# Kernel tuning notes

Measured on AMD Instinct MI355X. Metric: run time of the kernel, lower is better.

The kernel has to match this reference:

```python
import jax, jax.numpy as jnp
import numpy as np

HIDDEN = 512
HEAD = 64
SEQ = 2048
CHUNK = 256
GAMMA = 0.96875
SCALE_BASE = 512.0


def _xpos(x, downscale):
    # x: [B, L, hd]; XPOS with offset=0 (scale rows == length, no trimming needed)
    B, L, hd = x.shape
    half = hd // 2
    scale_vec = (jnp.arange(0, hd, 2, dtype=jnp.float32) + 0.4 * hd) / (1.4 * hd)  # [half]
    power = jnp.arange(L, dtype=jnp.float32) / SCALE_BASE                          # [L]
    scale = scale_vec[None, :] ** power[:, None]                                   # [L, half]
    inv_freq = 1.0 / (10000.0 ** (jnp.arange(half, dtype=jnp.float32) / half))
    sinusoid = jnp.arange(L, dtype=jnp.float32)[:, None] * inv_freq[None, :]       # [L, half]
    sin, cos = jnp.sin(sinusoid), jnp.cos(sinusoid)
    if downscale:
        scale = 1.0 / scale
    # duplicate_interleave: repeat each column twice -> [L, hd]
    sin_f = jnp.repeat(sin * scale, 2, axis=-1)
    cos_f = jnp.repeat(cos * scale, 2, axis=-1)
    x1 = x[:, :, 0::2]
    x2 = x[:, :, 1::2]
    rot = jnp.stack((-x2, x1), axis=-1).reshape(B, L, hd)  # rotate_every_two
    return x * cos_f + rot * sin_f


def _D_parallel():
    # D[i, j] = gamma^|i-j| if j < (i//chunk + 1)*chunk else 0 (block-causal with in-chunk lookahead)
    i = jnp.arange(SEQ)[:, None]
    j = jnp.arange(SEQ)[None, :]
    j_max = (i // CHUNK + 1) * CHUNK
    decay = GAMMA ** jnp.abs(i - j).astype(jnp.float32)
    return jnp.where(j < j_max, decay, 0.0)  # gamma>0 so no NaNs to scrub


def setup_inputs() -> dict:
    key = jax.random.key(0)
    k1, k2, k3, k4 = jax.random.split(key, 4)
    X = jax.random.normal(k1, (8, SEQ, HIDDEN), dtype=jnp.float32)
    W_Q = jax.random.normal(k2, (HIDDEN, HEAD), dtype=jnp.float32) / HIDDEN
    W_K = jax.random.normal(k3, (HIDDEN, HEAD), dtype=jnp.float32) / HIDDEN
    W_V = jax.random.normal(k4, (HIDDEN, HEAD), dtype=jnp.float32) / HIDDEN
    return {"X": X, "W_Q": W_Q, "W_K": W_K, "W_V": W_V}


def reference(X, W_Q, W_K, W_V):
    Q = _xpos(X @ W_Q, downscale=False)   # [B, S, H]
    K = _xpos(X @ W_K, downscale=True)    # [B, S, H]
    V = X @ W_V                           # [B, S, V]
    D = _D_parallel()                     # [S, S]
    scores = jnp.einsum('bqh,bkh->bqk', Q, K) * D[None]
    return jnp.einsum('bqk,bkv->bqv', scores, V)
```

## Files before the change

### kernel.cpp

```cpp
#include <hip/hip_runtime.h>
#include <hip/hip_bf16.h>


typedef __attribute__((ext_vector_type(8))) short short8;
typedef __attribute__((ext_vector_type(4))) float floatx4;

#define LOG2GAMMA (-0.04580350f)
#define GINV      (1.0f / 0.96875f)

static __device__ __forceinline__ unsigned short f2bf(float f) {
    __hip_bfloat16 h = __float2bfloat16(f);
    return *reinterpret_cast<unsigned short*>(&h);
}


__global__ __launch_bounds__(256) void prep_kernel(
    const float* __restrict__ Wq, const float* __restrict__ Wk,
    const float* __restrict__ Wv,
    __hip_bfloat16* __restrict__ Wfrag, float* __restrict__ tabs)
{
    int idx = blockIdx.x * 256 + threadIdx.x;
    const int WF_N = 192 * 512;
    if (idx < WF_N) {
        int j    = idx & 7;
        int n15  = (idx >> 3) & 15;
        int quad = (idx >> 7) & 3;
        int kkg  = (idx >> 9) & 15;
        int tile = idx >> 13;
        int n = tile * 16 + n15;
        int k = kkg * 32 + quad * 8 + j;
        int m = n >> 6, c = n & 63;
        const float* W = (m == 0) ? Wq : ((m == 1) ? Wk : Wv);
        Wfrag[idx] = __float2bfloat16(W[k * 64 + c]);
    } else {
        int t2 = idx - WF_N;
        if (t2 < 4 * 2048 * 32) {
            int tab = t2 >> 16;
            int rem = t2 & 65535;
            int pos = rem >> 5;
            int t   = rem & 31;
            float inv_freq = powf(10000.0f, -(float)t / 32.0f);
            float sinus = (float)pos * inv_freq;
            float s = sinf(sinus), c = cosf(sinus);
            float sv = (2.0f * (float)t + 0.4f * 64.0f) / (1.4f * 64.0f);
            float power = (float)pos / 512.0f;
            float scl = powf(sv, (tab >= 2) ? -power : power);
            tabs[t2] = ((tab & 1) == 0) ? c * scl : s * scl;
        }
    }
}

__global__ __launch_bounds__(256, 4) void proj_kernel(
    const float* __restrict__ X, const __hip_bfloat16* __restrict__ Wfrag,
    const float* __restrict__ tabs,
    __hip_bfloat16* __restrict__ Qfrag, __hip_bfloat16* __restrict__ Kfrag,
    __hip_bfloat16* __restrict__ Vfrag, __hip_bfloat16* __restrict__ Qsfrag,
    __hip_bfloat16* __restrict__ Ktfrag)
{
    __shared__ __hip_bfloat16 smem[32 * 520];

    int tid = threadIdx.x;
    int r0 = blockIdx.x * 32;
    int w = tid >> 6, lane = tid & 63, quad = lane >> 4, l15 = lane & 15;
    int rh = w & 1, nh = w >> 1;

#pragma unroll
    for (int u = 0; u < 16; u++) {
        int f = u * 256 + tid;
        int row = f >> 7, c = f & 127;
        float4 v = *(const float4*)(X + (r0 + row) * 512 + c * 4);
        ushort4 pk;
        pk.x = f2bf(v.x); pk.y = f2bf(v.y); pk.z = f2bf(v.z); pk.w = f2bf(v.w);
        *(ushort4*)&smem[row * 520 + c * 4] = pk;
    }
    __syncthreads();

    floatx4 acc[6];
#pragma unroll
    for (int t = 0; t < 6; t++) acc[t] = (floatx4){0.f, 0.f, 0.f, 0.f};

#pragma unroll
    for (int ks = 0; ks < 16; ks++) {
        short8 a = *(const short8*)&smem[(rh * 16 + l15) * 520 + ks * 32 + quad * 8];
#pragma unroll
        for (int t = 0; t < 6; t++) {
            int tile = nh * 6 + t;
            short8 bfr = *(const short8*)(Wfrag + ((tile * 16 + ks) * 64 + lane) * 8);
            acc[t] = __builtin_amdgcn_mfma_f32_16x16x32_bf16(a, bfr, acc[t], 0, 0, 0);
        }
    }
    __syncthreads();

    __hip_bfloat16* bufQ  = smem;
    __hip_bfloat16* bufK  = smem + 2304;
    __hip_bfloat16* bufV  = smem + 4608;
    __hip_bfloat16* bufQs = smem + 7168;
    int b = r0 >> 11, n0 = r0 & 2047;
    int rrow = rh * 16 + quad * 4;

#pragma unroll
    for (int tl = 0; tl < 6; tl++) {
        int t = nh * 6 + tl;
#pragma unroll
        for (int rg = 0; rg < 4; rg++) {
            int row = rrow + rg;
            int n = n0 + row;
            float val = acc[tl][rg];
            float prt = __shfl_xor(val, 1, 64);
            if (t < 4) {
                int ch = t * 16 + l15, tt = ch >> 1;
                float co = tabs[n * 32 + tt];
                float si = tabs[65536 + n * 32 + tt];
                float o = (l15 & 1) ? (val * co + prt * si) : (val * co - prt * si);
                bufQ[row * 72 + ch] = __float2bfloat16(o);
                float qs = exp2f(LOG2GAMMA * (float)((n & 255) + 1));
                bufQs[row * 72 + ch] = __float2bfloat16(o * qs);
            } else if (t < 8) {
                int ch = (t - 4) * 16 + l15, tt = ch >> 1;
                float co = tabs[131072 + n * 32 + tt];
                float si = tabs[196608 + n * 32 + tt];
                float o = (l15 & 1) ? (val * co + prt * si) : (val * co - prt * si);
                bufK[row * 72 + ch] = __float2bfloat16(o);
            } else {
                int ch = (t - 8) * 16 + l15;
                bufV[ch * 40 + row] = __float2bfloat16(val);
            }
        }
    }
    __syncthreads();

    {
        int tile2 = tid >> 7, kk = (tid >> 6) & 1, ln = tid & 63;
        int q2 = ln >> 4, m15 = ln & 15;
        size_t qkbase = ((((size_t)b * 128 + (n0 >> 4) + tile2) * 2 + kk) * 64 + ln) * 8;
        uint4 vq = *(const uint4*)&bufQ[(tile2 * 16 + m15) * 72 + kk * 32 + q2 * 8];
        *(uint4*)(Qfrag + qkbase) = vq;
        uint4 vqs = *(const uint4*)&bufQs[(tile2 * 16 + m15) * 72 + kk * 32 + q2 * 8];
        *(uint4*)(Qsfrag + qkbase) = vqs;
        uint4 vk = *(const uint4*)&bufK[(tile2 * 16 + m15) * 72 + kk * 32 + q2 * 8];
        *(uint4*)(Kfrag + qkbase) = vk;
        int t2 = tid >> 6;
        uint4 vv = *(const uint4*)&bufV[(t2 * 16 + m15) * 40 + q2 * 8];
        *(uint4*)(Vfrag + ((((size_t)b * 64 + (n0 >> 5)) * 4 + t2) * 64 + ln) * 8) = vv;
    }
    {
        int wdt = tid >> 6, ln2 = tid & 63;
        int q2 = ln2 >> 4, m15 = ln2 & 15;
        int jb0 = (n0 & 255) + q2 * 8;
        float sc = exp2f(LOG2GAMMA * (float)(255 - jb0));
        short8 pk;
#pragma unroll
        for (int jj = 0; jj < 8; jj++) {
            float v = __bfloat162float(bufK[(q2 * 8 + jj) * 72 + wdt * 16 + m15]) * sc;
            pk[jj] = (short)f2bf(v);
            sc *= GINV;
        }
        int c = n0 >> 8, ksg = (n0 >> 5) & 7;
        *(short8*)(Ktfrag + ((((size_t)(b * 8 + c) * 4 + wdt) * 8 + ksg) * 64 + ln2) * 8) = pk;
    }
}

__global__ __launch_bounds__(256, 2) void zk_kernel(
    const __hip_bfloat16* __restrict__ Ktfrag,
    const __hip_bfloat16* __restrict__ Vfrag, float* __restrict__ Zf)
{
    __shared__ float zz[64 * 68];

    int tid = threadIdx.x;
    int b = blockIdx.x >> 3, c = blockIdx.x & 7;
    int w = tid >> 6, lane = tid & 63, quad = lane >> 4, l15 = lane & 15;

    floatx4 acc[4];
#pragma unroll
    for (int t = 0; t < 4; t++) acc[t] = (floatx4){0.f, 0.f, 0.f, 0.f};

#pragma unroll
    for (int ks = 0; ks < 8; ks++) {
        short8 a = *(const short8*)(Ktfrag +
            ((((size_t)(b * 8 + c) * 4 + w) * 8 + ks) * 64 + lane) * 8);
#pragma unroll
        for (int vt = 0; vt < 4; vt++) {
            short8 bfr = *(const short8*)(Vfrag +
                ((((size_t)b * 64 + c * 8 + ks) * 4 + vt) * 64 + lane) * 8);
            acc[vt] = __builtin_amdgcn_mfma_f32_16x16x32_bf16(a, bfr, acc[vt], 0, 0, 0);
        }
    }
#pragma unroll
    for (int vt = 0; vt < 4; vt++)
#pragma unroll
        for (int rg = 0; rg < 4; rg++)
            zz[(w * 16 + quad * 4 + rg) * 68 + vt * 16 + l15] = acc[vt][rg];
    __syncthreads();

    {
        int vt = tid >> 6;
#pragma unroll
        for (int kk = 0; kk < 2; kk++) {
            float v[8];
#pragma unroll
            for (int jd = 0; jd < 8; jd++)
                v[jd] = zz[(kk * 32 + quad * 8 + jd) * 68 + vt * 16 + l15];
            float* zp = Zf + (((((size_t)(b * 8 + c) * 4 + vt) * 2 + kk) * 64 + lane) * 8);
            *(float4*)zp       = (float4){v[0], v[1], v[2], v[3]};
            *(float4*)(zp + 4) = (float4){v[4], v[5], v[6], v[7]};
        }
    }
}

__global__ __launch_bounds__(128, 4) void attn_kernel(
    const __hip_bfloat16* __restrict__ Qfrag, const __hip_bfloat16* __restrict__ Kfrag,
    const __hip_bfloat16* __restrict__ Vfrag, const __hip_bfloat16* __restrict__ Qsfrag,
    const float* __restrict__ Zf, float* __restrict__ out)
{
    __shared__ __hip_bfloat16 P[2 * 16 * 132];
    __shared__ float obuf[16 * 68];

    int tid = threadIdx.x;
    int b = blockIdx.x >> 7, qt = blockIdx.x & 127;
    int qc = qt >> 4;
    int h = tid >> 6, lane = tid & 63, quad = lane >> 4, l15 = lane & 15;
    __hip_bfloat16* Pw = P + h * 2112;

    short8 qf[2];
#pragma unroll
    for (int kk = 0; kk < 2; kk++)
        qf[kk] = *(const short8*)(Qfrag + (((size_t)(b * 128 + qt) * 2 + kk) * 64 + lane) * 8);

    floatx4 o[4];
#pragma unroll
    for (int t = 0; t < 4; t++) o[t] = (floatx4){0.f, 0.f, 0.f, 0.f};

    int il0 = (qt & 15) * 16 + quad * 4;

#pragma unroll
    for (int g = 0; g < 2; g++) {
        floatx4 s[4];
#pragma unroll
        for (int t = 0; t < 4; t++) s[t] = (floatx4){0.f, 0.f, 0.f, 0.f};
#pragma unroll
        for (int t = 0; t < 4; t++) {
            int kt = qc * 16 + h * 8 + g * 4 + t;
#pragma unroll
            for (int kk = 0; kk < 2; kk++) {
                short8 bfr = *(const short8*)(Kfrag +
                    (((size_t)(b * 128 + kt) * 2 + kk) * 64 + lane) * 8);
                s[t] = __builtin_amdgcn_mfma_f32_16x16x32_bf16(qf[kk], bfr, s[t], 0, 0, 0);
            }
        }
#pragma unroll
        for (int t = 0; t < 4; t++) {
            int jl = h * 128 + (g * 4 + t) * 16 + l15;
#pragma unroll
            for (int rg = 0; rg < 4; rg++) {
                int d = il0 + rg - jl; d = (d < 0) ? -d : d;
                float p = s[t][rg] * exp2f(LOG2GAMMA * (float)d);
                Pw[(quad * 4 + rg) * 132 + (g * 4 + t) * 16 + l15] = __float2bfloat16(p);
            }
        }
    }
#pragma unroll
    for (int ks = 0; ks < 4; ks++) {
        short8 a = *(const short8*)&Pw[l15 * 132 + ks * 32 + quad * 8];
#pragma unroll
        for (int vt = 0; vt < 4; vt++) {
            short8 bfr = *(const short8*)(Vfrag +
                ((((size_t)b * 64 + qc * 8 + h * 4 + ks) * 4 + vt) * 64 + lane) * 8);
            o[vt] = __builtin_amdgcn_mfma_f32_16x16x32_bf16(a, bfr, o[vt], 0, 0, 0);
        }
    }

    if (qc > 0) {
        short8 aq = *(const short8*)(Qsfrag +
            (((size_t)(b * 128 + qt) * 2 + h) * 64 + lane) * 8);
        int nz = (qc < 3) ? qc : 3;
        float cm0 = 1.0f;
        float cm1 = exp2f(LOG2GAMMA * 256.0f);
        float cm2 = exp2f(LOG2GAMMA * 512.0f);
#pragma unroll
        for (int vt = 0; vt < 4; vt++) {
            float hv[8];
#pragma unroll
            for (int jd = 0; jd < 8; jd++) hv[jd] = 0.f;
            for (int m = 0; m < nz; m++) {
                float cm = (m == 0) ? cm0 : ((m == 1) ? cm1 : cm2);
                const float* zp = Zf +
                    (((((size_t)(b * 8 + qc - 1 - m) * 4 + vt) * 2 + h) * 64 + lane) * 8);
                float4 z0 = *(const float4*)zp;
                float4 z1 = *(const float4*)(zp + 4);
                hv[0] += cm * z0.x; hv[1] += cm * z0.y;
                hv[2] += cm * z0.z; hv[3] += cm * z0.w;
                hv[4] += cm * z1.x; hv[5] += cm * z1.y;
                hv[6] += cm * z1.z; hv[7] += cm * z1.w;
            }
            short8 hb;
#pragma unroll
            for (int jd = 0; jd < 8; jd++) hb[jd] = (short)f2bf(hv[jd]);
            o[vt] = __builtin_amdgcn_mfma_f32_16x16x32_bf16(aq, hb, o[vt], 0, 0, 0);
        }
    }

    if (h == 1) {
#pragma unroll
        for (int vt = 0; vt < 4; vt++)
#pragma unroll
            for (int rg = 0; rg < 4; rg++)
                obuf[(quad * 4 + rg) * 68 + vt * 16 + l15] = o[vt][rg];
    }
    __syncthreads();
    if (h == 0) {
        int rbase = b * 2048 + qt * 16 + quad * 4;
#pragma unroll
        for (int vt = 0; vt < 4; vt++)
#pragma unroll
            for (int rg = 0; rg < 4; rg++)
                out[(size_t)(rbase + rg) * 64 + vt * 16 + l15] =
                    o[vt][rg] + obuf[(quad * 4 + rg) * 68 + vt * 16 + l15];
    }
}

extern "C" void kernel_launch(void* const* d_in, const int* in_sizes, int n_in,
                              void* d_out, int out_size, void* d_ws, size_t ws_size,
                              hipStream_t stream) {
    const float* X  = (const float*)d_in[0];
    const float* Wq = (const float*)d_in[1];
    const float* Wk = (const float*)d_in[2];
    const float* Wv = (const float*)d_in[3];
    float* out = (float*)d_out;

    char* ws = (char*)d_ws;
    __hip_bfloat16* Wfrag  = (__hip_bfloat16*)(ws);
    float*          tabs   = (float*)(ws + 196608);
    __hip_bfloat16* Qfrag  = (__hip_bfloat16*)(ws + 1245184);
    __hip_bfloat16* Kfrag  = (__hip_bfloat16*)(ws + 3342336);
    __hip_bfloat16* Vfrag  = (__hip_bfloat16*)(ws + 5439488);
    __hip_bfloat16* Qsfrag = (__hip_bfloat16*)(ws + 7536640);
    __hip_bfloat16* Ktfrag = (__hip_bfloat16*)(ws + 9633792);
    float*          Zf     = (float*)(ws + 11730944);

    prep_kernel<<<1408, 256, 0, stream>>>(Wq, Wk, Wv, Wfrag, tabs);
    proj_kernel<<<512, 256, 0, stream>>>(X, Wfrag, tabs, Qfrag, Kfrag, Vfrag,
                                         Qsfrag, Ktfrag);
    zk_kernel<<<64, 256, 0, stream>>>(Ktfrag, Vfrag, Zf);
    attn_kernel<<<1024, 128, 0, stream>>>(Qfrag, Kfrag, Vfrag, Qsfrag, Zf, out);
}
```

Measured before the change: 111.8 us.

## Drop Qs buffer, split zk over key halves, reuse A fragments in projection

Removes the separately stored decay-scaled Q copy. The cross-chunk term now uses the plain Q fragment and applies the per-row decay scale to the accumulator afterwards, which cuts proj_kernel stores and attn_kernel loads. The projection kernel has each wave cover both 16-row halves with 3 weight tiles, so each weight fragment load feeds two MFMAs. zk_kernel is split over two key halves to double its grid, and attn_kernel now reads and sums twice as many Z partials in exchange.

```diff
diff --git a/kernel.cpp b/kernel.cpp
--- a/kernel.cpp
+++ b/kernel.cpp
@@ -54,15 +54,13 @@
     const float* __restrict__ X, const __hip_bfloat16* __restrict__ Wfrag,
     const float* __restrict__ tabs,
     __hip_bfloat16* __restrict__ Qfrag, __hip_bfloat16* __restrict__ Kfrag,
-    __hip_bfloat16* __restrict__ Vfrag, __hip_bfloat16* __restrict__ Qsfrag,
-    __hip_bfloat16* __restrict__ Ktfrag)
+    __hip_bfloat16* __restrict__ Vfrag, __hip_bfloat16* __restrict__ Ktfrag)
 {
     __shared__ __hip_bfloat16 smem[32 * 520];
 
     int tid = threadIdx.x;
     int r0 = blockIdx.x * 32;
-    int w = tid >> 6, lane = tid & 63, quad = lane >> 4, l15 = lane & 15;
-    int rh = w & 1, nh = w >> 1;
+    int nh = tid >> 6, lane = tid & 63, quad = lane >> 4, l15 = lane & 15;
 
 #pragma unroll
     for (int u = 0; u < 16; u++) {
@@ -81,49 +79,50 @@
 
 #pragma unroll
     for (int ks = 0; ks < 16; ks++) {
-        short8 a = *(const short8*)&smem[(rh * 16 + l15) * 520 + ks * 32 + quad * 8];
-#pragma unroll
-        for (int t = 0; t < 6; t++) {
-            int tile = nh * 6 + t;
+        short8 a0 = *(const short8*)&smem[l15 * 520 + ks * 32 + quad * 8];
+        short8 a1 = *(const short8*)&smem[(16 + l15) * 520 + ks * 32 + quad * 8];
+#pragma unroll
+        for (int tl = 0; tl < 3; tl++) {
+            int tile = nh * 3 + tl;
             short8 bfr = *(const short8*)(Wfrag + ((tile * 16 + ks) * 64 + lane) * 8);
-            acc[t] = __builtin_amdgcn_mfma_f32_16x16x32_bf16(a, bfr, acc[t], 0, 0, 0);
-        }
-    }
-    __syncthreads();
-
-    __hip_bfloat16* bufQ  = smem;
-    __hip_bfloat16* bufK  = smem + 2304;
-    __hip_bfloat16* bufV  = smem + 4608;
-    __hip_bfloat16* bufQs = smem + 7168;
+            acc[tl * 2 + 0] = __builtin_amdgcn_mfma_f32_16x16x32_bf16(a0, bfr, acc[tl * 2 + 0], 0, 0, 0);
+            acc[tl * 2 + 1] = __builtin_amdgcn_mfma_f32_16x16x32_bf16(a1, bfr, acc[tl * 2 + 1], 0, 0, 0);
+        }
+    }
+    __syncthreads();
+
+    __hip_bfloat16* bufQ = smem;
+    __hip_bfloat16* bufK = smem + 2304;
+    __hip_bfloat16* bufV = smem + 4608;
     int b = r0 >> 11, n0 = r0 & 2047;
-    int rrow = rh * 16 + quad * 4;
-
-#pragma unroll
-    for (int tl = 0; tl < 6; tl++) {
-        int t = nh * 6 + tl;
-#pragma unroll
-        for (int rg = 0; rg < 4; rg++) {
-            int row = rrow + rg;
-            int n = n0 + row;
-            float val = acc[tl][rg];
-            float prt = __shfl_xor(val, 1, 64);
-            if (t < 4) {
-                int ch = t * 16 + l15, tt = ch >> 1;
-                float co = tabs[n * 32 + tt];
-                float si = tabs[65536 + n * 32 + tt];
-                float o = (l15 & 1) ? (val * co + prt * si) : (val * co - prt * si);
-                bufQ[row * 72 + ch] = __float2bfloat16(o);
-                float qs = exp2f(LOG2GAMMA * (float)((n & 255) + 1));
-                bufQs[row * 72 + ch] = __float2bfloat16(o * qs);
-            } else if (t < 8) {
-                int ch = (t - 4) * 16 + l15, tt = ch >> 1;
-                float co = tabs[131072 + n * 32 + tt];
-                float si = tabs[196608 + n * 32 + tt];
-                float o = (l15 & 1) ? (val * co + prt * si) : (val * co - prt * si);
-                bufK[row * 72 + ch] = __float2bfloat16(o);
-            } else {
-                int ch = (t - 8) * 16 + l15;
-                bufV[ch * 40 + row] = __float2bfloat16(val);
+
+#pragma unroll
+    for (int tl = 0; tl < 3; tl++) {
+        int t = nh * 3 + tl;
+#pragma unroll
+        for (int r = 0; r < 2; r++) {
+#pragma unroll
+            for (int rg = 0; rg < 4; rg++) {
+                int row = r * 16 + quad * 4 + rg;
+                int n = n0 + row;
+                float val = acc[tl * 2 + r][rg];
+                float prt = __shfl_xor(val, 1, 64);
+                if (t < 4) {
+                    int ch = t * 16 + l15, tt = ch >> 1;
+                    float co = tabs[n * 32 + tt];
+                    float si = tabs[65536 + n * 32 + tt];
+                    float o = (l15 & 1) ? (val * co + prt * si) : (val * co - prt * si);
+                    bufQ[row * 72 + ch] = __float2bfloat16(o);
+                } else if (t < 8) {
+                    int ch = (t - 4) * 16 + l15, tt = ch >> 1;
+                    float co = tabs[131072 + n * 32 + tt];
+                    float si = tabs[196608 + n * 32 + tt];
+                    float o = (l15 & 1) ? (val * co + prt * si) : (val * co - prt * si);
+                    bufK[row * 72 + ch] = __float2bfloat16(o);
+                } else {
+                    int ch = (t - 8) * 16 + l15;
+                    bufV[ch * 40 + row] = __float2bfloat16(val);
+                }
             }
         }
     }
@@ -135,8 +134,6 @@
         size_t qkbase = ((((size_t)b * 128 + (n0 >> 4) + tile2) * 2 + kk) * 64 + ln) * 8;
         uint4 vq = *(const uint4*)&bufQ[(tile2 * 16 + m15) * 72 + kk * 32 + q2 * 8];
         *(uint4*)(Qfrag + qkbase) = vq;
-        uint4 vqs = *(const uint4*)&bufQs[(tile2 * 16 + m15) * 72 + kk * 32 + q2 * 8];
-        *(uint4*)(Qsfrag + qkbase) = vqs;
         uint4 vk = *(const uint4*)&bufK[(tile2 * 16 + m15) * 72 + kk * 32 + q2 * 8];
         *(uint4*)(Kfrag + qkbase) = vk;
         int t2 = tid >> 6;
@@ -167,7 +164,7 @@
     __shared__ float zz[64 * 68];
 
     int tid = threadIdx.x;
-    int b = blockIdx.x >> 3, c = blockIdx.x & 7;
+    int b = blockIdx.x >> 4, c = (blockIdx.x >> 1) & 7, kh = blockIdx.x & 1;
     int w = tid >> 6, lane = tid & 63, quad = lane >> 4, l15 = lane & 15;
 
     floatx4 acc[4];
@@ -175,13 +172,14 @@
     for (int t = 0; t < 4; t++) acc[t] = (floatx4){0.f, 0.f, 0.f, 0.f};
 
 #pragma unroll
-    for (int ks = 0; ks < 8; ks++) {
+    for (int ks = 0; ks < 4; ks++) {
+        int ksg = kh * 4 + ks;
         short8 a = *(const short8*)(Ktfrag +
-            ((((size_t)(b * 8 + c) * 4 + w) * 8 + ks) * 64 + lane) * 8);
+            ((((size_t)(b * 8 + c) * 4 + w) * 8 + ksg) * 64 + lane) * 8);
 #pragma unroll
         for (int vt = 0; vt < 4; vt++) {
             short8 bfr = *(const short8*)(Vfrag +
-                ((((size_t)b * 64 + c * 8 + ks) * 4 + vt) * 64 + lane) * 8);
+                ((((size_t)b * 64 + c * 8 + ksg) * 4 + vt) * 64 + lane) * 8);
             acc[vt] = __builtin_amdgcn_mfma_f32_16x16x32_bf16(a, bfr, acc[vt], 0, 0, 0);
         }
     }
@@ -200,7 +198,8 @@
 #pragma unroll
             for (int jd = 0; jd < 8; jd++)
                 v[jd] = zz[(kk * 32 + quad * 8 + jd) * 68 + vt * 16 + l15];
-            float* zp = Zf + (((((size_t)(b * 8 + c) * 4 + vt) * 2 + kk) * 64 + lane) * 8);
+            float* zp = Zf +
+                ((((((size_t)(b * 8 + c) * 2 + kh) * 4 + vt) * 2 + kk) * 64 + lane) * 8);
             *(float4*)zp       = (float4){v[0], v[1], v[2], v[3]};
             *(float4*)(zp + 4) = (float4){v[4], v[5], v[6], v[7]};
         }
@@ -209,8 +208,8 @@
 
 __global__ __launch_bounds__(128, 4) void attn_kernel(
     const __hip_bfloat16* __restrict__ Qfrag, const __hip_bfloat16* __restrict__ Kfrag,
-    const __hip_bfloat16* __restrict__ Vfrag, const __hip_bfloat16* __restrict__ Qsfrag,
-    const float* __restrict__ Zf, float* __restrict__ out)
+    const __hip_bfloat16* __restrict__ Vfrag, const float* __restrict__ Zf,
+    float* __restrict__ out)
 {
     __shared__ __hip_bfloat16 P[2 * 16 * 132];
     __shared__ float obuf[16 * 68];
@@ -270,10 +269,10 @@
     }
 
     if (qc > 0) {
-        short8 aq = *(const short8*)(Qsfrag +
-            (((size_t)(b * 128 + qt) * 2 + h) * 64 + lane) * 8);
+        floatx4 oc[4];
+#pragma unroll
+        for (int t = 0; t < 4; t++) oc[t] = (floatx4){0.f, 0.f, 0.f, 0.f};
         int nz = (qc < 3) ? qc : 3;
-        float cm0 = 1.0f;
         float cm1 = exp2f(LOG2GAMMA * 256.0f);
         float cm2 = exp2f(LOG2GAMMA * 512.0f);
 #pragma unroll
@@ -282,21 +281,33 @@
 #pragma unroll
             for (int jd = 0; jd < 8; jd++) hv[jd] = 0.f;
             for (int m = 0; m < nz; m++) {
-                float cm = (m == 0) ? cm0 : ((m == 1) ? cm1 : cm2);
-                const float* zp = Zf +
-                    (((((size_t)(b * 8 + qc - 1 - m) * 4 + vt) * 2 + h) * 64 + lane) * 8);
-                float4 z0 = *(const float4*)zp;
-                float4 z1 = *(const float4*)(zp + 4);
-                hv[0] += cm * z0.x; hv[1] += cm * z0.y;
-                hv[2] += cm * z0.z; hv[3] += cm * z0.w;
-                hv[4] += cm * z1.x; hv[5] += cm * z1.y;
-                hv[6] += cm * z1.z; hv[7] += cm * z1.w;
+                float cm = (m == 0) ? 1.0f : ((m == 1) ? cm1 : cm2);
+#pragma unroll
+                for (int kh = 0; kh < 2; kh++) {
+                    const float* zp = Zf +
+                        ((((((size_t)(b * 8 + qc - 1 - m) * 2 + kh) * 4 + vt) * 2 + h) * 64 + lane) * 8);
+                    float4 z0 = *(const float4*)zp;
+                    float4 z1 = *(const float4*)(zp + 4);
+                    hv[0] += cm * z0.x; hv[1] += cm * z0.y;
+                    hv[2] += cm * z0.z; hv[3] += cm * z0.w;
+                    hv[4] += cm * z1.x; hv[5] += cm * z1.y;
+                    hv[6] += cm * z1.z; hv[7] += cm * z1.w;
+                }
             }
             short8 hb;
 #pragma unroll
             for (int jd = 0; jd < 8; jd++) hb[jd] = (short)f2bf(hv[jd]);
-            o[vt] = __builtin_amdgcn_mfma_f32_16x16x32_bf16(aq, hb, o[vt], 0, 0, 0);
-        }
+            oc[vt] = __builtin_amdgcn_mfma_f32_16x16x32_bf16(qf[h], hb, oc[vt], 0, 0, 0);
+        }
+        float rs[4];
+#pragma unroll
+        for (int rg = 0; rg < 4; rg++)
+            rs[rg] = exp2f(LOG2GAMMA * (float)(il0 + rg + 1));
+#pragma unroll
+        for (int vt = 0; vt < 4; vt++)
+#pragma unroll
+            for (int rg = 0; rg < 4; rg++)
+                o[vt][rg] += oc[vt][rg] * rs[rg];
     }
 
     if (h == 1) {
@@ -333,13 +344,11 @@
     __hip_bfloat16* Qfrag  = (__hip_bfloat16*)(ws + 1245184);
     __hip_bfloat16* Kfrag  = (__hip_bfloat16*)(ws + 3342336);
     __hip_bfloat16* Vfrag  = (__hip_bfloat16*)(ws + 5439488);
-    __hip_bfloat16* Qsfrag = (__hip_bfloat16*)(ws + 7536640);
-    __hip_bfloat16* Ktfrag = (__hip_bfloat16*)(ws + 9633792);
-    float*          Zf     = (float*)(ws + 11730944);
+    __hip_bfloat16* Ktfrag = (__hip_bfloat16*)(ws + 7536640);
+    float*          Zf     = (float*)(ws + 9633792);
 
     prep_kernel<<<1408, 256, 0, stream>>>(Wq, Wk, Wv, Wfrag, tabs);
-    proj_kernel<<<512, 256, 0, stream>>>(X, Wfrag, tabs, Qfrag, Kfrag, Vfrag,
-                                         Qsfrag, Ktfrag);
-    zk_kernel<<<64, 256, 0, stream>>>(Ktfrag, Vfrag, Zf);
-    attn_kernel<<<1024, 128, 0, stream>>>(Qfrag, Kfrag, Vfrag, Qsfrag, Zf, out);
-}
+    proj_kernel<<<512, 256, 0, stream>>>(X, Wfrag, tabs, Qfrag, Kfrag, Vfrag, Ktfrag);
+    zk_kernel<<<128, 256, 0, stream>>>(Ktfrag, Vfrag, Zf);
+    attn_kernel<<<1024, 128, 0, stream>>>(Qfrag, Kfrag, Vfrag, Zf, out);
+}
```

Measured after the change: 111.5 us. About the same (-0.3%).
